# Performance work log

Hardware: AMD Instinct MI355X
Metric: run time of the kernel (lower is better)

Reference implementation:

```python
import jax, jax.numpy as jnp
import numpy as np

D_MODEL, N_HEADS, D_FF = 512, 8, 2048
D_K = D_MODEL // N_HEADS
EPS = 1e-5


def layer_norm(x, g, b):
    mu = jnp.mean(x, axis=-1, keepdims=True)
    var = jnp.mean(jnp.square(x - mu), axis=-1, keepdims=True)
    return (x - mu) * jax.lax.rsqrt(var + EPS) * g + b


def setup_inputs() -> dict:
    key = jax.random.key(0)
    ks = jax.random.split(key, 12)
    B, S = 2, 2048
    s_attn = 1.0 / np.sqrt(D_MODEL)
    s_ff1 = 1.0 / np.sqrt(D_MODEL)
    s_ff2 = 1.0 / np.sqrt(D_FF)
    inp = {
        "x": jax.random.normal(ks[0], (B, S, D_MODEL), dtype=jnp.float32),
        "mask": jnp.ones((B, 1, 1, S), dtype=jnp.int32),
        "Wq": jax.random.normal(ks[1], (D_MODEL, D_MODEL), jnp.float32) * s_attn,
        "bq": jnp.zeros((D_MODEL,), jnp.float32),
        "Wk": jax.random.normal(ks[2], (D_MODEL, D_MODEL), jnp.float32) * s_attn,
        "bk": jnp.zeros((D_MODEL,), jnp.float32),
        "Wv": jax.random.normal(ks[3], (D_MODEL, D_MODEL), jnp.float32) * s_attn,
        "bv": jnp.zeros((D_MODEL,), jnp.float32),
        "Wo": jax.random.normal(ks[4], (D_MODEL, D_MODEL), jnp.float32) * s_attn,
        "bo": jnp.zeros((D_MODEL,), jnp.float32),
        "W1": jax.random.normal(ks[5], (D_MODEL, D_FF), jnp.float32) * s_ff1,
        "b1": jnp.zeros((D_FF,), jnp.float32),
        "W2": jax.random.normal(ks[6], (D_FF, D_MODEL), jnp.float32) * s_ff2,
        "b2": jnpp.zeros((D_MODEL,), jnp.float32) if False else jnp.zeros((D_MODEL,), jnp.float32),
        "g1": jnp.ones((D_MODEL,), jnp.float32),
        "beta1": jnp.zeros((D_MODEL,), jnp.float32),
        "g2": jnp.ones((D_MODEL,), jnp.float32),
        "beta2": jnp.zeros((D_MODEL,), jnp.float32),
    }
    return inp


def reference(x, mask, Wq, bq, Wk, bk, Wv, bv, Wo, bo, W1, b1, W2, b2, g1, beta1, g2, beta2):
    B, S, _ = x.shape
    # projections -> [B, H, S, Dk]
    def split_heads(t):
        return t.reshape(B, S, N_HEADS, D_K).transpose(0, 2, 1, 3)
    q = split_heads(x @ Wq + bq)
    k = split_heads(x @ Wk + bk)
    v = split_heads(x @ Wv + bv)
    scores = jnp.einsum("bhqd,bhkd->bhqk", q, k) / np.sqrt(D_K)
    scores = jnp.where(mask == 0, jnp.float32(-1e9), scores)
    attn = jax.nn.softmax(scores, axis=-1)
    ctx = jnp.einsum("bhqk,bhkd->bhqd", attn, v)
    ctx = ctx.transpose(0, 2, 1, 3).reshape(B, S, D_MODEL)
    attn_out = ctx @ Wo + bo
    x1 = layer_norm(x + attn_out, g1, beta1)
    ff = jax.nn.relu(x1 @ W1 + b1) @ W2 + b2
    return layer_norm(x1 + ff, g2, beta2)
```

## Files before the change

### kernel.cpp

```cpp
#include <hip/hip_runtime.h>
#include <hip/hip_bf16.h>


#define D_MODEL 512
#define N_HEADS 8
#define D_K 64
#define D_FF 2048
#define BATCH 2
#define SEQ 2048
#define NROWS (BATCH * SEQ)

typedef __hip_bfloat16 bf16;
typedef __attribute__((ext_vector_type(8))) short bf16x8;
typedef __attribute__((ext_vector_type(4))) float f32x4;

__device__ __forceinline__ unsigned short f2b(float f) {
  union { bf16 b; unsigned short u; } cv;
  cv.b = __float2bfloat16(f);
  return cv.u;
}
__device__ __forceinline__ float b2f(unsigned short u) {
  return __uint_as_float(((unsigned int)u) << 16);
}
__device__ __forceinline__ float toF(const bf16 x) { return __bfloat162float(x); }
__device__ __forceinline__ float toF(const float x) { return x; }
__device__ __forceinline__ void storeC(float* p, float v) { *p = v; }
__device__ __forceinline__ void storeC(bf16* p, float v) {
  *p = __float2bfloat16(v);
}

__device__ __forceinline__ void ld8f(const float* p, float* v) {
  const float4 a = *(const float4*)p;
  const float4 b = *(const float4*)(p + 4);
  v[0] = a.x; v[1] = a.y; v[2] = a.z; v[3] = a.w;
  v[4] = b.x; v[5] = b.y; v[6] = b.z; v[7] = b.w;
}
__device__ __forceinline__ void ld8f(const bf16* p, float* v) {
  const bf16x8 u = *(const bf16x8*)p;
#pragma unroll
  for (int i = 0; i < 8; ++i) v[i] = b2f((unsigned short)u[i]);
}
__device__ __forceinline__ void st8f(float* p, const float* v) {
  *(float4*)p = make_float4(v[0], v[1], v[2], v[3]);
  *(float4*)(p + 4) = make_float4(v[4], v[5], v[6], v[7]);
}
__device__ __forceinline__ void st8f(bf16* p, const float* v) {
  bf16x8 u;
#pragma unroll
  for (int i = 0; i < 8; ++i) u[i] = (short)f2b(v[i]);
  *(bf16x8*)p = u;
}

#define WT_Q 0
#define WT_K 262144
#define WT_V 524288
#define WT_O 786432
#define WT_1 1048576
#define WT_2 2097152

__global__ __launch_bounds__(256) void prep_kernel(
    const float* __restrict__ Wq, const float* __restrict__ Wk,
    const float* __restrict__ Wv, const float* __restrict__ Wo,
    const float* __restrict__ W1, const float* __restrict__ W2,
    bf16* __restrict__ outw, const float* __restrict__ x,
    bf16* __restrict__ xb) {
  const int z = blockIdx.z;
  const int t = threadIdx.x;

  if (z == 6) {
    const size_t base =
        ((size_t)(blockIdx.y * 32 + blockIdx.x) * 2048) + (size_t)t * 8;
    float v[8];
    ld8f(x + base, v);
    st8f(xb + base, v);
    return;
  }

  const float* W;
  int R, Cn;
  size_t off;
  if (z == 0)      { W = Wq; R = 512;  Cn = 512;  off = WT_Q; }
  else if (z == 1) { W = Wk; R = 512;  Cn = 512;  off = WT_K; }
  else if (z == 2) { W = Wv; R = 512;  Cn = 512;  off = WT_V; }
  else if (z == 3) { W = Wo; R = 512;  Cn = 512;  off = WT_O; }
  else if (z == 4) { W = W1; R = 512;  Cn = 2048; off = WT_1; }
  else             { W = W2; R = 2048; Cn = 512;  off = WT_2; }
  const int c0 = blockIdx.x * 64;
  const int r0 = blockIdx.y * 64;
  if (c0 >= Cn || r0 >= R) return;

  __shared__ short tile[64][72];
  {
    const int r = t >> 2, cg = (t & 3) * 16;
    const float* src = &W[(size_t)(r0 + r) * Cn + c0 + cg];
#pragma unroll
    for (int i = 0; i < 4; ++i) {
      const float4 v = *(const float4*)(src + 4 * i);
      tile[cg + 4 * i + 0][r] = (short)f2b(v.x);
      tile[cg + 4 * i + 1][r] = (short)f2b(v.y);
      tile[cg + 4 * i + 2][r] = (short)f2b(v.z);
      tile[cg + 4 * i + 3][r] = (short)f2b(v.w);
    }
  }
  __syncthreads();
  {
    const int c = t >> 2, rg = (t & 3) * 16;
    short* dst = (short*)outw + off + (size_t)(c0 + c) * R + r0 + rg;
    *(bf16x8*)dst = *(const bf16x8*)&tile[c][rg];
    *(bf16x8*)(dst + 8) = *(const bf16x8*)&tile[c][rg + 8];
  }
}

template <int BM, int BN, bool RELU, bool RESID>
__global__ __launch_bounds__(256) void gemm_bf16_kernel(
    const bf16* __restrict__ A, int lda,
    const bf16* __restrict__ Wt0, const bf16* __restrict__ Wt1,
    const bf16* __restrict__ Wt2, int ldk,
    const float* __restrict__ b0, const float* __restrict__ b1,
    const float* __restrict__ b2,
    bf16* __restrict__ C0, bf16* __restrict__ C1, bf16* __restrict__ C2,
    int ldc, int K, const bf16* __restrict__ R) {
  const bf16* Wt = (blockIdx.z == 0) ? Wt0 : (blockIdx.z == 1 ? Wt1 : Wt2);
  const float* bias = (blockIdx.z == 0) ? b0 : (blockIdx.z == 1 ? b1 : b2);
  bf16* C = (blockIdx.z == 0) ? C0 : (blockIdx.z == 1 ? C1 : C2);

  constexpr int WX = BN / 64;
  constexpr int WY = 4 / WX;
  constexpr int RG = BM / (16 * WY);
  constexpr int NA = BM / 32;
  constexpr int NW = BN / 32;

  __shared__ short as_[BM][72];
  __shared__ short bs[BN][72];

  const int rowBase = blockIdx.y * BM;
  const int colBase = blockIdx.x * BN;
  const int t = threadIdx.x;
  const int wave = t >> 6;
  const int lane = t & 63;
  const int quad = lane >> 4;
  const int l15 = lane & 15;
  const int wy = wave / WX;
  const int wx = wave % WX;

  const int arow = (NA == 2) ? (t >> 2) : (t >> 1);
  const int akc = (NA == 2) ? ((t & 3) * 16) : ((t & 1) * 32);
  const int wrow = (NW == 2) ? (t >> 2) : (t >> 1);
  const int wkc = (NW == 2) ? ((t & 3) * 16) : ((t & 1) * 32);

  const short* Abase = (const short*)A + (size_t)(rowBase + arow) * lda + akc;
  const short* Wbase = (const short*)Wt + (size_t)(colBase + wrow) * ldk + wkc;

  bf16x8 areg[NA], wreg[NW];
#pragma unroll
  for (int i = 0; i < NA; ++i) areg[i] = *(const bf16x8*)(Abase + 8 * i);
#pragma unroll
  for (int i = 0; i < NW; ++i) wreg[i] = *(const bf16x8*)(Wbase + 8 * i);

  f32x4 acc[RG][4];
#pragma unroll
  for (int i = 0; i < RG; ++i)
#pragma unroll
    for (int nt = 0; nt < 4; ++nt) acc[i][nt] = (f32x4){0.f, 0.f, 0.f, 0.f};

  for (int k0 = 0; k0 < K; k0 += 64) {
#pragma unroll
    for (int i = 0; i < NA; ++i) *(bf16x8*)&as_[arow][akc + 8 * i] = areg[i];
#pragma unroll
    for (int i = 0; i < NW; ++i) *(bf16x8*)&bs[wrow][wkc + 8 * i] = wreg[i];

    if (k0 + 64 < K) {
#pragma unroll
      for (int i = 0; i < NA; ++i)
        areg[i] = *(const bf16x8*)(Abase + k0 + 64 + 8 * i);
#pragma unroll
      for (int i = 0; i < NW; ++i)
        wreg[i] = *(const bf16x8*)(Wbase + k0 + 64 + 8 * i);
    }
    __syncthreads();

#pragma unroll
    for (int kc = 0; kc < 2; ++kc) {
      bf16x8 af[RG];
#pragma unroll
      for (int i = 0; i < RG; ++i)
        af[i] = *(const bf16x8*)
            &as_[wy * (16 * RG) + i * 16 + l15][quad * 8 + kc * 32];
#pragma unroll
      for (int nt = 0; nt < 4; ++nt) {
        const bf16x8 bfr = *(const bf16x8*)
            &bs[wx * 64 + nt * 16 + l15][quad * 8 + kc * 32];
#pragma unroll
        for (int i = 0; i < RG; ++i)
          acc[i][nt] = __builtin_amdgcn_mfma_f32_16x16x32_bf16(
              af[i], bfr, acc[i][nt], 0, 0, 0);
      }
    }
    __syncthreads();
  }

#pragma unroll
  for (int i = 0; i < RG; ++i)
#pragma unroll
    for (int nt = 0; nt < 4; ++nt) {
      const int col = colBase + wx * 64 + nt * 16 + l15;
#pragma unroll
      for (int r = 0; r < 4; ++r) {
        const int row = rowBase + wy * (16 * RG) + i * 16 + quad * 4 + r;
        float v = acc[i][nt][r] + bias[col];
        if (RESID) v += toF(R[(size_t)row * ldc + col]);
        if (RELU) v = fmaxf(v, 0.f);
        storeC(&C[(size_t)row * ldc + col], v);
      }
    }
}

__global__ __launch_bounds__(512) void attn_mfma_kernel(
    const bf16* __restrict__ Q, const bf16* __restrict__ Km,
    const bf16* __restrict__ V, const int* __restrict__ mask,
    bf16* __restrict__ ctx) {
  const int qt = blockIdx.x;
  const int bh = blockIdx.y;
  const int b = bh >> 3;
  const int h = bh & 7;
  const int t = threadIdx.x;
  const int wave = t >> 6;
  const int half = wave >> 2;
  const int wq = wave & 3;
  const int lane = t & 63;
  const int quad = lane >> 4;
  const int l15 = lane & 15;

  __shared__ __align__(16) char smem[74240];
  auto ks = (short(*)[64][72])(smem);
  auto vt = (short(*)[64][72])(smem + 18432);
  auto pb = (short(*)[32][72])(smem + 36864);
  auto mk = (int(*)[64])(smem + 73728);
  auto mg = (float(*)[32][68])(smem);

  bf16x8 qf[2][2];
#pragma unroll
  for (int rg = 0; rg < 2; ++rg) {
    const short* qg = (const short*)Q +
        (size_t)(b * SEQ + qt * 128 + wq * 32 + rg * 16 + l15) * D_MODEL +
        h * D_K + quad * 8;
    qf[rg][0] = *(const bf16x8*)qg;
    qf[rg][1] = *(const bf16x8*)(qg + 32);
  }

  f32x4 of[2][4];
#pragma unroll
  for (int rg = 0; rg < 2; ++rg)
#pragma unroll
    for (int nt = 0; nt < 4; ++nt) of[rg][nt] = (f32x4){0.f, 0.f, 0.f, 0.f};
  float l_acc[2][4] = {{0.f, 0.f, 0.f, 0.f}, {0.f, 0.f, 0.f, 0.f}};

  const int hs = t >> 8;
  const int tt = t & 255;
  const int kr = tt >> 2, kc0 = (tt & 3) * 16;
  const int vk = tt & 63, vc0 = ((tt >> 6) & 3) * 16;

  bf16x8 kv0, kv1, vv0, vv1;
  int mv = 1;
  {
    const int keyRow = (hs * 16 + 0) * 64;
    const short* kg = (const short*)Km +
        (size_t)(b * SEQ + keyRow + kr) * D_MODEL + h * D_K + kc0;
    kv0 = *(const bf16x8*)kg;
    kv1 = *(const bf16x8*)(kg + 8);
    const short* vg = (const short*)V +
        (size_t)(b * SEQ + keyRow + vk) * D_MODEL + h * D_K + vc0;
    vv0 = *(const bf16x8*)vg;
    vv1 = *(const bf16x8*)(vg + 8);
    if (tt < 64) mv = mask[b * SEQ + keyRow + tt];
  }

  for (int kt = 0; kt < 16; ++kt) {
    *(bf16x8*)&ks[hs][kr][kc0] = kv0;
    *(bf16x8*)&ks[hs][kr][kc0 + 8] = kv1;
#pragma unroll
    for (int i = 0; i < 8; ++i) vt[hs][vc0 + i][vk] = vv0[i];
#pragma unroll
    for (int i = 0; i < 8; ++i) vt[hs][vc0 + 8 + i][vk] = vv1[i];
    if (tt < 64) mk[hs][tt] = mv;

    if (kt + 1 < 16) {
      const int keyRow = (hs * 16 + kt + 1) * 64;
      const short* kg = (const short*)Km +
          (size_t)(b * SEQ + keyRow + kr) * D_MODEL + h * D_K + kc0;
      kv0 = *(const bf16x8*)kg;
      kv1 = *(const bf16x8*)(kg + 8);
      const short* vg = (const short*)V +
          (size_t)(b * SEQ + keyRow + vk) * D_MODEL + h * D_K + vc0;
      vv0 = *(const bf16x8*)vg;
      vv1 = *(const bf16x8*)(vg + 8);
      if (tt < 64) mv = mask[b * SEQ + keyRow + tt];
    }
    __syncthreads();

    f32x4 sf[2][4];
#pragma unroll
    for (int nt = 0; nt < 4; ++nt) {
      const bf16x8 kf0 = *(const bf16x8*)&ks[half][l15 + 16 * nt][quad * 8];
      const bf16x8 kf1 =
          *(const bf16x8*)&ks[half][l15 + 16 * nt][quad * 8 + 32];
#pragma unroll
      for (int rg = 0; rg < 2; ++rg) {
        f32x4 acc = (f32x4){0.f, 0.f, 0.f, 0.f};
        acc = __builtin_amdgcn_mfma_f32_16x16x32_bf16(qf[rg][0], kf0, acc, 0, 0, 0);
        acc = __builtin_amdgcn_mfma_f32_16x16x32_bf16(qf[rg][1], kf1, acc, 0, 0, 0);
        sf[rg][nt] = acc;
      }
    }

#pragma unroll
    for (int nt = 0; nt < 4; ++nt) {
      const bool dead = (mk[half][l15 + 16 * nt] == 0);
#pragma unroll
      for (int rg = 0; rg < 2; ++rg)
#pragma unroll
        for (int r = 0; r < 4; ++r) {
          float p = __expf(fmaf(sf[rg][nt][r], 0.125f, -8.f));
          if (dead) p = 0.f;
          l_acc[rg][r] += p;
          pb[wave][rg * 16 + quad * 4 + r][l15 + 16 * nt] = (short)f2b(p);
        }
    }

#pragma unroll
    for (int kc = 0; kc < 2; ++kc) {
      bf16x8 pf[2];
#pragma unroll
      for (int rg = 0; rg < 2; ++rg)
        pf[rg] = *(const bf16x8*)&pb[wave][rg * 16 + l15][kc * 32 + quad * 8];
#pragma unroll
      for (int nt = 0; nt < 4; ++nt) {
        const bf16x8 vf =
            *(const bf16x8*)&vt[half][l15 + 16 * nt][kc * 32 + quad * 8];
#pragma unroll
        for (int rg = 0; rg < 2; ++rg)
          of[rg][nt] = __builtin_amdgcn_mfma_f32_16x16x32_bf16(
              pf[rg], vf, of[rg][nt], 0, 0, 0);
      }
    }
    __syncthreads();
  }

#pragma unroll
  for (int xm = 1; xm < 16; xm <<= 1)
#pragma unroll
    for (int rg = 0; rg < 2; ++rg)
#pragma unroll
      for (int r = 0; r < 4; ++r)
        l_acc[rg][r] += __shfl_xor(l_acc[rg][r], xm, 64);

#pragma unroll
  for (int rg = 0; rg < 2; ++rg)
#pragma unroll
    for (int nt = 0; nt < 4; ++nt)
#pragma unroll
      for (int r = 0; r < 4; ++r)
        mg[wave][rg * 16 + quad * 4 + r][l15 + 16 * nt] = of[rg][nt][r];
  if (l15 == 0) {
#pragma unroll
    for (int rg = 0; rg < 2; ++rg)
#pragma unroll
      for (int r = 0; r < 4; ++r)
        mg[wave][rg * 16 + quad * 4 + r][64] = l_acc[rg][r];
  }
  __syncthreads();

  if (wave < 4) {
    const int pw = wave + 4;
#pragma unroll
    for (int rg = 0; rg < 2; ++rg)
#pragma unroll
      for (int r = 0; r < 4; ++r) {
        const int qrow = rg * 16 + quad * 4 + r;
        const float inv = 1.f / (l_acc[rg][r] + mg[pw][qrow][64]);
        const int row = qt * 128 + wave * 32 + qrow;
        bf16* cp = ctx + (size_t)(b * SEQ + row) * D_MODEL + h * D_K;
#pragma unroll
        for (int nt = 0; nt < 4; ++nt)
          cp[l15 + 16 * nt] = __float2bfloat16(
              (of[rg][nt][r] + mg[pw][qrow][l15 + 16 * nt]) * inv);
      }
  }
}

template <typename BT, typename OT>
__global__ __launch_bounds__(256) void ln_kernel(
    const BT* __restrict__ base, const float* __restrict__ g,
    const float* __restrict__ beta, OT* __restrict__ out) {
  const int wave = threadIdx.x >> 6;
  const int lane = threadIdx.x & 63;
  const int row = blockIdx.x * 4 + wave;
  const size_t rb = (size_t)row * D_MODEL + lane * 8;

  float v[8];
  ld8f(base + rb, v);

  float s = 0.f;
#pragma unroll
  for (int i = 0; i < 8; ++i) s += v[i];
#pragma unroll
  for (int xm = 1; xm < 64; xm <<= 1) s += __shfl_xor(s, xm, 64);
  const float mu = s * (1.f / (float)D_MODEL);

  float q = 0.f;
#pragma unroll
  for (int i = 0; i < 8; ++i) {
    v[i] -= mu;
    q += v[i] * v[i];
  }
#pragma unroll
  for (int xm = 1; xm < 64; xm <<= 1) q += __shfl_xor(q, xm, 64);
  const float rs = rsqrtf(q * (1.f / (float)D_MODEL) + 1e-5f);

  float gv[8], bv[8];
  ld8f(g + lane * 8, gv);
  ld8f(beta + lane * 8, bv);
#pragma unroll
  for (int i = 0; i < 8; ++i) v[i] = v[i] * rs * gv[i] + bv[i];
  st8f(out + rb, v);
}

extern "C" void kernel_launch(void* const* d_in, const int* in_sizes, int n_in,
                              void* d_out, int out_size, void* d_ws, size_t ws_size,
                              hipStream_t stream) {
  const float* x     = (const float*)d_in[0];
  const int*   mask  = (const int*)d_in[1];
  const float* Wq    = (const float*)d_in[2];
  const float* bq    = (const float*)d_in[3];
  const float* Wk    = (const float*)d_in[4];
  const float* bk    = (const float*)d_in[5];
  const float* Wv    = (const float*)d_in[6];
  const float* bv    = (const float*)d_in[7];
  const float* Wo    = (const float*)d_in[8];
  const float* bo    = (const float*)d_in[9];
  const float* W1    = (const float*)d_in[10];
  const float* b1    = (const float*)d_in[11];
  const float* W2    = (const float*)d_in[12];
  const float* b2    = (const float*)d_in[13];
  const float* g1    = (const float*)d_in[14];
  const float* beta1 = (const float*)d_in[15];
  const float* g2    = (const float*)d_in[16];
  const float* beta2 = (const float*)d_in[17];
  float* out = (float*)d_out;

  char* ws = (char*)d_ws;
  const size_t MB4 = (size_t)NROWS * D_MODEL * sizeof(bf16);
  bf16* q        = (bf16*)(ws + 0 * MB4);
  bf16* kbuf     = (bf16*)(ws + 1 * MB4);
  bf16* vbuf     = (bf16*)(ws + 2 * MB4);
  bf16* ctx      = (bf16*)(ws + 3 * MB4);
  bf16* xb       = (bf16*)(ws + 4 * MB4);
  bf16* attn_out = q;
  bf16* x1       = kbuf;
  bf16* ffacc    = vbuf;
  bf16* ffmid    = (bf16*)(ws + 4 * MB4);

  bf16* wt = (bf16*)d_out;

  const dim3 blk(256);

  prep_kernel<<<dim3(32, 32, 7), blk, 0, stream>>>(Wq, Wk, Wv, Wo, W1, W2, wt,
                                                   x, xb);

  gemm_bf16_kernel<128, 128, false, false>
      <<<dim3(D_MODEL / 128, NROWS / 128, 3), blk, 0, stream>>>(
          xb, D_MODEL, wt + WT_Q, wt + WT_K, wt + WT_V, D_MODEL,
          bq, bk, bv, q, kbuf, vbuf, D_MODEL, D_MODEL, nullptr);

  attn_mfma_kernel<<<dim3(SEQ / 128, BATCH * N_HEADS), dim3(512), 0, stream>>>(
      q, kbuf, vbuf, mask, ctx);

  gemm_bf16_kernel<128, 64, false, true>
      <<<dim3(D_MODEL / 64, NROWS / 128, 1), blk, 0, stream>>>(
          ctx, D_MODEL, wt + WT_O, wt + WT_O, wt + WT_O, D_MODEL,
          bo, bo, bo, attn_out, attn_out, attn_out, D_MODEL, D_MODEL, xb);

  ln_kernel<bf16, bf16><<<NROWS / 4, blk, 0, stream>>>(attn_out, g1, beta1, x1);

  gemm_bf16_kernel<128, 128, true, false>
      <<<dim3(D_FF / 128, NROWS / 128, 1), blk, 0, stream>>>(
          x1, D_MODEL, wt + WT_1, wt + WT_1, wt + WT_1, D_MODEL,
          b1, b1, b1, ffmid, ffmid, ffmid, D_FF, D_MODEL, nullptr);

  gemm_bf16_kernel<128, 64, false, true>
      <<<dim3(D_MODEL / 64, NROWS / 128, 1), blk, 0, stream>>>(
          ffmid, D_FF, wt + WT_2, wt + WT_2, wt + WT_2, D_FF,
          b2, b2, b2, ffacc, ffacc, ffacc, D_MODEL, D_FF, x1);

  ln_kernel<bf16, float><<<NROWS / 4, blk, 0, stream>>>(ffacc, g2, beta2, out);
}
```

Baseline: 207.3 us.

## Split attention keys four ways with 64-row query tiles; shrink output GEMM tiles

After: 210.1 us. Within noise of the previous version (+1.4%).

```diff
diff --git a/kernel.cpp b/kernel.cpp
--- a/kernel.cpp
+++ b/kernel.cpp
@@ -225,24 +225,24 @@
   const int h = bh & 7;
   const int t = threadIdx.x;
   const int wave = t >> 6;
-  const int half = wave >> 2;
-  const int wq = wave & 3;
+  const int qd = wave >> 1;
+  const int wq = wave & 1;
   const int lane = t & 63;
   const int quad = lane >> 4;
   const int l15 = lane & 15;
 
-  __shared__ __align__(16) char smem[74240];
-  auto ks = (short(*)[64][72])(smem);
-  auto vt = (short(*)[64][72])(smem + 18432);
-  auto pb = (short(*)[32][72])(smem + 36864);
-  auto mk = (int(*)[64])(smem + 73728);
+  __shared__ __align__(16) char smem[69632];
+  auto ks = (short(*)[32][72])(smem);
+  auto vt = (short(*)[64][40])(smem + 18432);
+  auto pb = (short(*)[32][40])(smem + 38912);
+  auto mk = (int(*)[32])(smem + 59392);
   auto mg = (float(*)[32][68])(smem);
 
   bf16x8 qf[2][2];
 #pragma unroll
   for (int rg = 0; rg < 2; ++rg) {
     const short* qg = (const short*)Q +
-        (size_t)(b * SEQ + qt * 128 + wq * 32 + rg * 16 + l15) * D_MODEL +
+        (size_t)(b * SEQ + qt * 64 + wq * 32 + rg * 16 + l15) * D_MODEL +
         h * D_K + quad * 8;
     qf[rg][0] = *(const bf16x8*)qg;
     qf[rg][1] = *(const bf16x8*)(qg + 32);
@@ -255,15 +255,15 @@
     for (int nt = 0; nt < 4; ++nt) of[rg][nt] = (f32x4){0.f, 0.f, 0.f, 0.f};
   float l_acc[2][4] = {{0.f, 0.f, 0.f, 0.f}, {0.f, 0.f, 0.f, 0.f}};
 
-  const int hs = t >> 8;
-  const int tt = t & 255;
+  const int hs = t >> 7;
+  const int tt = t & 127;
   const int kr = tt >> 2, kc0 = (tt & 3) * 16;
-  const int vk = tt & 63, vc0 = ((tt >> 6) & 3) * 16;
+  const int vk = tt & 31, vc0 = (tt >> 5) * 16;
 
   bf16x8 kv0, kv1, vv0, vv1;
   int mv = 1;
   {
-    const int keyRow = (hs * 16 + 0) * 64;
+    const int keyRow = hs * 512;
     const short* kg = (const short*)Km +
         (size_t)(b * SEQ + keyRow + kr) * D_MODEL + h * D_K + kc0;
     kv0 = *(const bf16x8*)kg;
@@ -272,7 +272,7 @@
         (size_t)(b * SEQ + keyRow + vk) * D_MODEL + h * D_K + vc0;
     vv0 = *(const bf16x8*)vg;
     vv1 = *(const bf16x8*)(vg + 8);
-    if (tt < 64) mv = mask[b * SEQ + keyRow + tt];
+    if (tt < 32) mv = mask[b * SEQ + keyRow + tt];
   }
 
   for (int kt = 0; kt < 16; ++kt) {
@@ -282,10 +282,10 @@
     for (int i = 0; i < 8; ++i) vt[hs][vc0 + i][vk] = vv0[i];
 #pragma unroll
     for (int i = 0; i < 8; ++i) vt[hs][vc0 + 8 + i][vk] = vv1[i];
-    if (tt < 64) mk[hs][tt] = mv;
+    if (tt < 32) mk[hs][tt] = mv;
 
     if (kt + 1 < 16) {
-      const int keyRow = (hs * 16 + kt + 1) * 64;
+      const int keyRow = hs * 512 + (kt + 1) * 32;
       const short* kg = (const short*)Km +
           (size_t)(b * SEQ + keyRow + kr) * D_MODEL + h * D_K + kc0;
       kv0 = *(const bf16x8*)kg;
@@ -294,16 +294,15 @@
           (size_t)(b * SEQ + keyRow + vk) * D_MODEL + h * D_K + vc0;
       vv0 = *(const bf16x8*)vg;
       vv1 = *(const bf16x8*)(vg + 8);
-      if (tt < 64) mv = mask[b * SEQ + keyRow + tt];
+      if (tt < 32) mv = mask[b * SEQ + keyRow + tt];
     }
     __syncthreads();
 
-    f32x4 sf[2][4];
-#pragma unroll
-    for (int nt = 0; nt < 4; ++nt) {
-      const bf16x8 kf0 = *(const bf16x8*)&ks[half][l15 + 16 * nt][quad * 8];
-      const bf16x8 kf1 =
-          *(const bf16x8*)&ks[half][l15 + 16 * nt][quad * 8 + 32];
+    f32x4 sf[2][2];
+#pragma unroll
+    for (int nt = 0; nt < 2; ++nt) {
+      const bf16x8 kf0 = *(const bf16x8*)&ks[qd][l15 + 16 * nt][quad * 8];
+      const bf16x8 kf1 = *(const bf16x8*)&ks[qd][l15 + 16 * nt][quad * 8 + 32];
 #pragma unroll
       for (int rg = 0; rg < 2; ++rg) {
         f32x4 acc = (f32x4){0.f, 0.f, 0.f, 0.f};
@@ -314,8 +313,8 @@
     }
 
 #pragma unroll
-    for (int nt = 0; nt < 4; ++nt) {
-      const bool dead = (mk[half][l15 + 16 * nt] == 0);
+    for (int nt = 0; nt < 2; ++nt) {
+      const bool dead = (mk[qd][l15 + 16 * nt] == 0);
 #pragma unroll
       for (int rg = 0; rg < 2; ++rg)
 #pragma unroll
@@ -327,16 +326,14 @@
         }
     }
 
-#pragma unroll
-    for (int kc = 0; kc < 2; ++kc) {
+    {
       bf16x8 pf[2];
 #pragma unroll
       for (int rg = 0; rg < 2; ++rg)
-        pf[rg] = *(const bf16x8*)&pb[wave][rg * 16 + l15][kc * 32 + quad * 8];
+        pf[rg] = *(const bf16x8*)&pb[wave][rg * 16 + l15][quad * 8];
 #pragma unroll
       for (int nt = 0; nt < 4; ++nt) {
-        const bf16x8 vf =
-            *(const bf16x8*)&vt[half][l15 + 16 * nt][kc * 32 + quad * 8];
+        const bf16x8 vf = *(const bf16x8*)&vt[qd][l15 + 16 * nt][quad * 8];
 #pragma unroll
         for (int rg = 0; rg < 2; ++rg)
           of[rg][nt] = __builtin_amdgcn_mfma_f32_16x16x32_bf16(
@@ -370,20 +367,26 @@
   }
   __syncthreads();
 
-  if (wave < 4) {
-    const int pw = wave + 4;
+  if (wave < 2) {
 #pragma unroll
     for (int rg = 0; rg < 2; ++rg)
 #pragma unroll
       for (int r = 0; r < 4; ++r) {
         const int qrow = rg * 16 + quad * 4 + r;
-        const float inv = 1.f / (l_acc[rg][r] + mg[pw][qrow][64]);
-        const int row = qt * 128 + wave * 32 + qrow;
+        float lt = l_acc[rg][r];
+#pragma unroll
+        for (int i = 1; i < 4; ++i) lt += mg[wave + 2 * i][qrow][64];
+        const float inv = 1.f / lt;
+        const int row = qt * 64 + wave * 32 + qrow;
         bf16* cp = ctx + (size_t)(b * SEQ + row) * D_MODEL + h * D_K;
 #pragma unroll
-        for (int nt = 0; nt < 4; ++nt)
-          cp[l15 + 16 * nt] = __float2bfloat16(
-              (of[rg][nt][r] + mg[pw][qrow][l15 + 16 * nt]) * inv);
+        for (int nt = 0; nt < 4; ++nt) {
+          float o = of[rg][nt][r];
+#pragma unroll
+          for (int i = 1; i < 4; ++i)
+            o += mg[wave + 2 * i][qrow][l15 + 16 * nt];
+          cp[l15 + 16 * nt] = __float2bfloat16(o * inv);
+        }
       }
   }
 }
@@ -472,11 +475,11 @@
           xb, D_MODEL, wt + WT_Q, wt + WT_K, wt + WT_V, D_MODEL,
           bq, bk, bv, q, kbuf, vbuf, D_MODEL, D_MODEL, nullptr);
 
-  attn_mfma_kernel<<<dim3(SEQ / 128, BATCH * N_HEADS), dim3(512), 0, stream>>>(
+  attn_mfma_kernel<<<dim3(SEQ / 64, BATCH * N_HEADS), dim3(512), 0, stream>>>(
       q, kbuf, vbuf, mask, ctx);
 
-  gemm_bf16_kernel<128, 64, false, true>
-      <<<dim3(D_MODEL / 64, NROWS / 128, 1), blk, 0, stream>>>(
+  gemm_bf16_kernel<64, 64, false, true>
+      <<<dim3(D_MODEL / 64, NROWS / 64, 1), blk, 0, stream>>>(
           ctx, D_MODEL, wt + WT_O, wt + WT_O, wt + WT_O, D_MODEL,
           bo, bo, bo, attn_out, attn_out, attn_out, D_MODEL, D_MODEL, xb);
 
@@ -487,8 +490,8 @@
           x1, D_MODEL, wt + WT_1, wt + WT_1, wt + WT_1, D_MODEL,
           b1, b1, b1, ffmid, ffmid, ffmid, D_FF, D_MODEL, nullptr);
 
-  gemm_bf16_kernel<128, 64, false, true>
-      <<<dim3(D_MODEL / 64, NROWS / 128, 1), blk, 0, stream>>>(
+  gemm_bf16_kernel<64, 64, false, true>
+      <<<dim3(D_MODEL / 64, NROWS / 64, 1), blk, 0, stream>>>(
           ffmid, D_FF, wt + WT_2, wt + WT_2, wt + WT_2, D_FF,
           b2, b2, b2, ffacc, ffacc, ffacc, D_MODEL, D_FF, x1);
 
```
